# Performance work log

Measured on AMD Instinct MI355X. Metric: run time of the kernel, lower is better.

## Reference

```python
import jax, jax.numpy as jnp
import numpy as np

NUM_HEADS = 16


def _bayes_w(mu, rho, eps):
    # reparameterized weight sample: w = mu + softplus(rho) * eps
    return mu + jax.nn.softplus(rho) * eps


def setup_inputs() -> dict:
    key = jax.random.key(0)
    ks = jax.random.split(key, 12)
    B, N, C = 4, 2048, 1024
    x = jax.random.normal(ks[0], (B, N, C), jnp.float32)
    w_scale = 0.02
    q_w = jax.random.normal(ks[1], (C, C), jnp.float32) * w_scale
    k_w = jax.random.normal(ks[2], (C, C), jnp.float32) * w_scale
    v_mu = jax.random.normal(ks[3], (C, C), jnp.float32) * w_scale
    v_rho = jax.random.normal(ks[4], (C, C), jnp.float32) * 0.1 - 3.0
    v_eps = jax.random.normal(ks[5], (C, C), jnp.float32)
    proj_mu = jax.random.normal(ks[6], (C, C), jnp.float32) * w_scale
    proj_rho = jax.random.normal(ks[7], (C, C), jnp.float32) * 0.1 - 3.0
    proj_eps = jax.random.normal(ks[8], (C, C), jnp.float32)
    pb_mu = jax.random.normal(ks[9], (C,), jnp.float32) * w_scale
    pb_rho = jax.random.normal(ks[10], (C,), jnp.float32) * 0.1 - 3.0
    pb_eps = jax.random.normal(ks[11], (C,), jnp.float32)
    return {"x": x, "q_w": q_w, "k_w": k_w, "v_mu": v_mu, "v_rho": v_rho,
            "v_eps": v_eps, "proj_mu": proj_mu, "proj_rho": proj_rho,
            "proj_eps": proj_eps, "pb_mu": pb_mu, "pb_rho": pb_rho,
            "pb_eps": pb_eps}


def reference(x, q_w, k_w, v_mu, v_rho, v_eps, proj_mu, proj_rho, proj_eps,
              pb_mu, pb_rho, pb_eps):
    B, N, C = x.shape
    H = NUM_HEADS
    D = C // H
    scale = D ** -0.5
    v_w = _bayes_w(v_mu, v_rho, v_eps)
    # projections (torch Linear: y = x @ W.T)
    q = (x @ q_w.T).reshape(B, N, H, D).transpose(0, 2, 1, 3)  # [B,H,N,D]
    k = (x @ k_w.T).reshape(B, N, H, D).transpose(0, 2, 1, 3)
    v = (x @ v_w.T).reshape(B, N, H, D).transpose(0, 2, 1, 3)
    attn = jax.nn.softmax(jnp.einsum("bhnd,bhmd->bhnm", q * scale, k), axis=-1)
    out = jnp.einsum("bhnm,bhmd->bhnd", attn, v)
    out = out.transpose(0, 2, 1, 3).reshape(B, N, C)
    p_w = _bayes_w(proj_mu, proj_rho, proj_eps)
    p_b = _bayes_w(pb_mu, pb_rho, pb_eps)
    return out @ p_w.T + p_b
```

## Files before the change

### kernel.cpp

```cpp
#include <hip/hip_runtime.h>
#include <hip/hip_bf16.h>
#include <cstdint>
#include <math.h>

typedef __bf16 bf16;
typedef __bf16 bf16x8 __attribute__((ext_vector_type(8)));
typedef __bf16 bf16x4 __attribute__((ext_vector_type(4)));
typedef float  f32x4 __attribute__((ext_vector_type(4)));

#define LOG2E 1.4426950408889634f

#if __has_builtin(__builtin_amdgcn_exp2f)
#define EXP2(x) __builtin_amdgcn_exp2f(x)
#else
#define EXP2(x) exp2f(x)
#endif

#define AS1 __attribute__((address_space(1)))
#define AS3 __attribute__((address_space(3)))

__device__ __forceinline__ void gload_lds16(const bf16* g, bf16* l) {
    __builtin_amdgcn_global_load_lds((AS1 void*)g, (AS3 void*)l, 16, 0, 0);
}

__device__ __forceinline__ float softplus_f(float r) {
    return (r > 15.f) ? r : log1pf(expf(r));
}

#define MFMA16(a, b, c) __builtin_amdgcn_mfma_f32_16x16x32_bf16((a), (b), (c), 0, 0, 0)
#define CFENCE asm volatile("" ::: "memory")

__global__ __launch_bounds__(256)
void prep_kernel(const float* __restrict__ x, bf16* __restrict__ xb,
                 const float* __restrict__ q_w, const float* __restrict__ k_w,
                 bf16* __restrict__ wqkv,
                 const float* __restrict__ v_mu, const float* __restrict__ v_rho,
                 const float* __restrict__ v_eps,
                 const float* __restrict__ p_mu, const float* __restrict__ p_rho,
                 const float* __restrict__ p_eps, bf16* __restrict__ pwb,
                 const float* __restrict__ pb_mu, const float* __restrict__ pb_rho,
                 const float* __restrict__ pb_eps, float* __restrict__ p_b) {
    const int Wsz = 1024 * 1024;
    int blk = blockIdx.x;
    if (blk < 8192) {
        int i = blk * 256 + threadIdx.x;
        float4 v = ((const float4*)x)[i];
        bf16 o[4] = {(bf16)v.x, (bf16)v.y, (bf16)v.z, (bf16)v.w};
        *(uint64_t*)&xb[i * 4] = *(uint64_t*)o;
    } else if (blk < 10240) {
        const float* src = (blk < 9216) ? q_w : k_w;
        bf16* dst = (blk < 9216) ? wqkv : wqkv + Wsz;
        int i = ((blk - 8192) & 1023) * 256 + threadIdx.x;
        float4 v = ((const float4*)src)[i];
        bf16 o[4] = {(bf16)v.x, (bf16)v.y, (bf16)v.z, (bf16)v.w};
        *(uint64_t*)&dst[i * 4] = *(uint64_t*)o;
    } else if (blk < 12288) {
        const bool isv = blk < 11264;
        const float* mu  = isv ? v_mu  : p_mu;
        const float* rho = isv ? v_rho : p_rho;
        const float* eps = isv ? v_eps : p_eps;
        bf16* dst = isv ? wqkv + 2 * Wsz : pwb;
        int i = ((blk - 10240) & 1023) * 256 + threadIdx.x;
        float4 m = ((const float4*)mu)[i];
        float4 r = ((const float4*)rho)[i];
        float4 e = ((const float4*)eps)[i];
        bf16 o[4] = {(bf16)(m.x + softplus_f(r.x) * e.x),
                     (bf16)(m.y + softplus_f(r.y) * e.y),
                     (bf16)(m.z + softplus_f(r.z) * e.z),
                     (bf16)(m.w + softplus_f(r.w) * e.w)};
        *(uint64_t*)&dst[i * 4] = *(uint64_t*)o;
    } else {
        int i = threadIdx.x;
        float4 m = ((const float4*)pb_mu)[i];
        float4 r = ((const float4*)pb_rho)[i];
        float4 e = ((const float4*)pb_eps)[i];
        float4 o;
        o.x = m.x + softplus_f(r.x) * e.x;
        o.y = m.y + softplus_f(r.y) * e.y;
        o.z = m.z + softplus_f(r.z) * e.z;
        o.w = m.w + softplus_f(r.w) * e.w;
        ((float4*)p_b)[i] = o;
    }
}

template <typename OutT>
__global__ __launch_bounds__(512, 2)
void gemm_8ph(const bf16* __restrict__ A, const bf16* __restrict__ W,
              OutT* __restrict__ C, const float* __restrict__ bias,
              int M, int N, int K, float q_scale, int q_cols) {
    __shared__ bf16 sA[2][256 * 64];
    __shared__ bf16 sB[2][256 * 64];

    const int lane  = threadIdx.x & 63;
    const int wv    = threadIdx.x >> 6;
    const int wr    = wv >> 2;
    const int wc    = wv & 3;
    const int col16 = lane & 15, quad = lane >> 4;

    const int nwg = gridDim.x * gridDim.y;
    int bidl = blockIdx.y * gridDim.x + blockIdx.x;
    if ((nwg & 7) == 0) bidl = (bidl & 7) * (nwg >> 3) + (bidl >> 3);
    const int m0 = (bidl / gridDim.x) * 256;
    const int n0 = (bidl % gridDim.x) * 256;

    const int st_r = lane >> 2;
    const int st_c = ((lane & 3) * 8) ^ (((lane >> 5) & 1) << 4);
    const bf16* Asrc = A + (size_t)(m0 + st_r) * K + st_c;
    const bf16* Bsrc = W + (size_t)(n0 + st_r) * K + st_c;
    const size_t rgK = (size_t)16 * K;

    const int lp = col16 * 32 + ((quad * 8) ^ (((col16 >> 3) & 1) << 4));

    f32x4 acc[2][2][4][2] = {};
    const int NT = K >> 6;

    {
        const bf16* sa0 = Asrc + (size_t)wv * rgK;
        const bf16* sb0 = Bsrc + (size_t)wv * rgK;
        const bf16* sa1 = Asrc + (size_t)(8 + wv) * rgK;
        const bf16* sb1 = Bsrc + (size_t)(8 + wv) * rgK;
        gload_lds16(sa0,      &sA[0][wv * 1024]);        gload_lds16(sa0 + 32, &sA[0][wv * 1024 + 512]);
        gload_lds16(sb0,      &sB[0][wv * 1024]);        gload_lds16(sb0 + 32, &sB[0][wv * 1024 + 512]);
        gload_lds16(sa1,      &sA[0][(8+wv) * 1024]);    gload_lds16(sa1 + 32, &sA[0][(8+wv) * 1024 + 512]);
        gload_lds16(sb1,      &sB[0][(8+wv) * 1024]);    gload_lds16(sb1 + 32, &sB[0][(8+wv) * 1024 + 512]);
        gload_lds16(sa0 + 64, &sA[1][wv * 1024]);        gload_lds16(sa0 + 96, &sA[1][wv * 1024 + 512]);
        gload_lds16(sb0 + 64, &sB[1][wv * 1024]);        gload_lds16(sb0 + 96, &sB[1][wv * 1024 + 512]);
    }
    asm volatile("s_waitcnt vmcnt(4)" ::: "memory");
    __builtin_amdgcn_s_barrier();
    CFENCE;

    for (int t = 0; t < NT; ++t) {
        const int d = t & 1;
        const int k1 = (t + 1) << 6, k2 = (t + 2) << 6;
        bf16x8 afr[4][2], bfr[2][2];

#pragma unroll
        for (int mm = 0; mm < 4; ++mm)
#pragma unroll
            for (int ks = 0; ks < 2; ++ks)
                afr[mm][ks] = *(const bf16x8*)&sA[d][((2*mm + wr) * 2 + ks) * 512 + lp];
#pragma unroll
        for (int nn = 0; nn < 2; ++nn)
#pragma unroll
            for (int ks = 0; ks < 2; ++ks)
                bfr[nn][ks] = *(const bf16x8*)&sB[d][((nn*4 + wc) * 2 + ks) * 512 + lp];
        if (t + 1 < NT) {
            const bf16* s = Asrc + (size_t)(8 + wv) * rgK + k1;
            bf16* l = &sA[d ^ 1][(8 + wv) * 1024];
            gload_lds16(s, l); gload_lds16(s + 32, l + 512);
        }
        __builtin_amdgcn_s_setprio(1);
#pragma unroll
        for (int mm = 0; mm < 4; ++mm)
#pragma unroll
            for (int nn = 0; nn < 2; ++nn) {
                acc[0][0][mm][nn] = MFMA16(afr[mm][0], bfr[nn][0], acc[0][0][mm][nn]);
                acc[0][0][mm][nn] = MFMA16(afr[mm][1], bfr[nn][1], acc[0][0][mm][nn]);
            }
        __builtin_amdgcn_s_setprio(0);
        CFENCE; __builtin_amdgcn_s_barrier(); CFENCE;

#pragma unroll
        for (int nn = 0; nn < 2; ++nn)
#pragma unroll
            for (int ks = 0; ks < 2; ++ks)
                bfr[nn][ks] = *(const bf16x8*)&sB[d][((8 + nn*4 + wc) * 2 + ks) * 512 + lp];
        if (t + 1 < NT) {
            const bf16* s = Bsrc + (size_t)(8 + wv) * rgK + k1;
            bf16* l = &sB[d ^ 1][(8 + wv) * 1024];
            gload_lds16(s, l); gload_lds16(s + 32, l + 512);
        }
        __builtin_amdgcn_s_setprio(1);
#pragma unroll
        for (int mm = 0; mm < 4; ++mm)
#pragma unroll
            for (int nn = 0; nn < 2; ++nn) {
                acc[0][1][mm][nn] = MFMA16(afr[mm][0], bfr[nn][0], acc[0][1][mm][nn]);
                acc[0][1][mm][nn] = MFMA16(afr[mm][1], bfr[nn][1], acc[0][1][mm][nn]);
            }
        __builtin_amdgcn_s_setprio(0);
        CFENCE; __builtin_amdgcn_s_barrier(); CFENCE;

#pragma unroll
        for (int mm = 0; mm < 4; ++mm)
#pragma unroll
            for (int ks = 0; ks < 2; ++ks)
                afr[mm][ks] = *(const bf16x8*)&sA[d][((8 + 2*mm + wr) * 2 + ks) * 512 + lp];
#pragma unroll
        for (int nn = 0; nn < 2; ++nn)
#pragma unroll
            for (int ks = 0; ks < 2; ++ks)
                bfr[nn][ks] = *(const bf16x8*)&sB[d][((nn*4 + wc) * 2 + ks) * 512 + lp];
        if (t + 2 < NT) {
            const bf16* s = Asrc + (size_t)wv * rgK + k2;
            bf16* l = &sA[d][wv * 1024];
            gload_lds16(s, l); gload_lds16(s + 32, l + 512);
        }
        __builtin_amdgcn_s_setprio(1);
#pragma unroll
        for (int mm = 0; mm < 4; ++mm)
#pragma unroll
            for (int nn = 0; nn < 2; ++nn) {
                acc[1][0][mm][nn] = MFMA16(afr[mm][0], bfr[nn][0], acc[1][0][mm][nn]);
                acc[1][0][mm][nn] = MFMA16(afr[mm][1], bfr[nn][1], acc[1][0][mm][nn]);
            }
        __builtin_amdgcn_s_setprio(0);
        CFENCE; __builtin_amdgcn_s_barrier(); CFENCE;

#pragma unroll
        for (int nn = 0; nn < 2; ++nn)
#pragma unroll
            for (int ks = 0; ks < 2; ++ks)
                bfr[nn][ks] = *(const bf16x8*)&sB[d][((8 + nn*4 + wc) * 2 + ks) * 512 + lp];
        if (t + 2 < NT) {
            const bf16* s = Bsrc + (size_t)wv * rgK + k2;
            bf16* l = &sB[d][wv * 1024];
            gload_lds16(s, l); gload_lds16(s + 32, l + 512);
        }
        __builtin_amdgcn_s_setprio(1);
#pragma unroll
        for (int mm = 0; mm < 4; ++mm)
#pragma unroll
            for (int nn = 0; nn < 2; ++nn) {
                acc[1][1][mm][nn] = MFMA16(afr[mm][0], bfr[nn][0], acc[1][1][mm][nn]);
                acc[1][1][mm][nn] = MFMA16(afr[mm][1], bfr[nn][1], acc[1][1][mm][nn]);
            }
        __builtin_amdgcn_s_setprio(0);
        if (t + 2 < NT) asm volatile("s_waitcnt vmcnt(4)" ::: "memory");
        else            asm volatile("s_waitcnt vmcnt(0)" ::: "memory");
        __builtin_amdgcn_s_barrier();
        CFENCE;
    }

    const float scale = (n0 < q_cols) ? q_scale : 1.0f;
#pragma unroll
    for (int a = 0; a < 2; ++a)
#pragma unroll
        for (int b = 0; b < 2; ++b)
#pragma unroll
            for (int mm = 0; mm < 4; ++mm)
#pragma unroll
                for (int nn = 0; nn < 2; ++nn) {
                    int row = m0 + (a * 8 + 2 * mm + wr) * 16 + quad * 4;
                    int cc  = n0 + (b * 8 + nn * 4 + wc) * 16 + col16;
                    float bv = bias ? bias[cc] : 0.f;
#pragma unroll
                    for (int r = 0; r < 4; ++r)
                        C[(size_t)(row + r) * N + cc] = (OutT)(acc[a][b][mm][nn][r] * scale + bv);
                }
}

#define SWZ(row, ec) ((row) * 64 + ((ec) ^ (((row) & 7) << 3)))

__global__ __launch_bounds__(256, 2)
void attn_kernel(const bf16* __restrict__ QKV, bf16* __restrict__ O) {
    __shared__ bf16 sK[2][64 * 64];
    __shared__ bf16 sVt[64 * 64];
    __shared__ bf16 sP [256 * 64];

    const int lane = threadIdx.x & 63;
    const int wv   = threadIdx.x >> 6;
    const int col  = lane & 15, quad = lane >> 4;

    const int bid  = blockIdx.x;
    const int work = (bid & 7) * 64 + (bid >> 3);
    const int qt = work & 7, h = (work >> 3) & 15, b = work >> 7;

    const size_t rowQ0 = (size_t)b * 2048 + qt * 256;
    const bf16* Qg = QKV + rowQ0 * 3072 + h * 64;
    const bf16* Kg = QKV + (size_t)b * 2048 * 3072 + 1024 + h * 64;
    const bf16* Vg = QKV + (size_t)b * 2048 * 3072 + 2048 + h * 64;

    const int rloc = lane >> 3;
    const bf16* Kdma = Kg + (size_t)(wv * 16 + rloc) * 3072 + (((lane & 7) ^ rloc) * 8);

    gload_lds16(Kdma,                    &sK[0][(wv * 16) * 64]);
    gload_lds16(Kdma + (size_t)8 * 3072, &sK[0][(wv * 16 + 8) * 64]);

    const int dc0 = wv * 8, dc1 = 32 + wv * 8;
    bf16x8 vr0 = *(const bf16x8*)&Vg[(size_t)lane * 3072 + dc0];
    bf16x8 vr1 = *(const bf16x8*)&Vg[(size_t)lane * 3072 + dc1];

#pragma unroll
    for (int it = 0; it < 8; ++it) {
        int c = it * 256 + threadIdx.x;
        int row = c >> 3, ec = (c & 7) * 8;
        *(bf16x8*)&sP[SWZ(row, ec)] = *(const bf16x8*)&Qg[(size_t)row * 3072 + ec];
    }
    __syncthreads();
    bf16x8 qf[4][2];
#pragma unroll
    for (int mi = 0; mi < 4; ++mi)
#pragma unroll
        for (int ks = 0; ks < 2; ++ks)
            qf[mi][ks] = *(const bf16x8*)&sP[SWZ(wv * 64 + mi * 16 + col, ks * 32 + quad * 8)];

    f32x4 lsum[4] = {};
    f32x4 o[4][4] = {};
    const int cx = col & 7;

    for (int t = 0; t < 32; ++t) {
        const int p = t & 1;

#pragma unroll
        for (int j = 0; j < 8; ++j) sVt[SWZ(dc0 + j, lane)] = vr0[j];
#pragma unroll
        for (int j = 0; j < 8; ++j) sVt[SWZ(dc1 + j, lane)] = vr1[j];
        __syncthreads();

        if (t < 31) {
            const bf16* kn = Kdma + (size_t)(t * 64 + 64) * 3072;
            gload_lds16(kn,                    &sK[p ^ 1][(wv * 16) * 64]);
            gload_lds16(kn + (size_t)8 * 3072, &sK[p ^ 1][(wv * 16 + 8) * 64]);
        }

        bf16x8 kf0[4], kf1[4];
#pragma unroll
        for (int nj = 0; nj < 4; ++nj) {
            kf0[nj] = *(const bf16x8*)&sK[p][(nj * 16 + col) * 64 + ((quad ^ cx) * 8)];
            kf1[nj] = *(const bf16x8*)&sK[p][(nj * 16 + col) * 64 + (((quad ^ cx) ^ 4) * 8)];
        }

#pragma unroll
        for (int mi = 0; mi < 4; ++mi) {
            f32x4 st[4];
            __builtin_amdgcn_s_setprio(1);
#pragma unroll
            for (int nj = 0; nj < 4; ++nj) {
                f32x4 tacc = {0.f, 0.f, 0.f, 0.f};
                tacc = MFMA16(kf0[nj], qf[mi][0], tacc);
                tacc = MFMA16(kf1[nj], qf[mi][1], tacc);
                st[nj] = tacc;
            }
            __builtin_amdgcn_s_setprio(0);
#pragma unroll
            for (int nj = 0; nj < 4; ++nj) {
                f32x4 pv;
#pragma unroll
                for (int r = 0; r < 4; ++r) pv[r] = EXP2(st[nj][r]);
                lsum[mi] += pv;
                bf16x4 pk = {(bf16)pv[0], (bf16)pv[1], (bf16)pv[2], (bf16)pv[3]};
                *(bf16x4*)&sP[SWZ(wv * 64 + mi * 16 + col, nj * 16 + quad * 4)] = pk;
            }
        }

        if (t < 31) {
            const bf16* vn = Vg + (size_t)(t * 64 + 64 + lane) * 3072;
            vr0 = *(const bf16x8*)&vn[dc0];
            vr1 = *(const bf16x8*)&vn[dc1];
        }

        __builtin_amdgcn_s_setprio(1);
#pragma unroll
        for (int ks = 0; ks < 2; ++ks) {
            bf16x8 pf[4];
#pragma unroll
            for (int mi = 0; mi < 4; ++mi)
                pf[mi] = *(const bf16x8*)&sP[SWZ(wv * 64 + mi * 16 + col, ks * 32 + quad * 8)];
#pragma unroll
            for (int dj = 0; dj < 4; ++dj) {
                bf16x8 vf = *(const bf16x8*)&sVt[SWZ(dj * 16 + col, ks * 32 + quad * 8)];
#pragma unroll
                for (int mi = 0; mi < 4; ++mi)
                    o[mi][dj] = MFMA16(pf[mi], vf, o[mi][dj]);
            }
        }
        __builtin_amdgcn_s_setprio(0);
        __syncthreads();
    }

#pragma unroll
    for (int mi = 0; mi < 4; ++mi) {
        float l = lsum[mi][0] + lsum[mi][1] + lsum[mi][2] + lsum[mi][3];
        l += __shfl_xor(l, 16, 64);
        l += __shfl_xor(l, 32, 64);
#pragma unroll
        for (int r = 0; r < 4; ++r) {
            float inv = 1.f / __shfl(l, quad * 4 + r, 64);
            size_t row = rowQ0 + wv * 64 + mi * 16 + quad * 4 + r;
#pragma unroll
            for (int dj = 0; dj < 4; ++dj)
                O[row * 1024 + h * 64 + dj * 16 + col] = (bf16)(o[mi][dj][r] * inv);
        }
    }
}

extern "C" void kernel_launch(void* const* d_in, const int* in_sizes, int n_in,
                              void* d_out, int out_size, void* d_ws, size_t ws_size,
                              hipStream_t stream) {
    const float* x      = (const float*)d_in[0];
    const float* q_w    = (const float*)d_in[1];
    const float* k_w    = (const float*)d_in[2];
    const float* v_mu   = (const float*)d_in[3];
    const float* v_rho  = (const float*)d_in[4];
    const float* v_eps  = (const float*)d_in[5];
    const float* p_mu   = (const float*)d_in[6];
    const float* p_rho  = (const float*)d_in[7];
    const float* p_eps  = (const float*)d_in[8];
    const float* pb_mu  = (const float*)d_in[9];
    const float* pb_rho = (const float*)d_in[10];
    const float* pb_eps = (const float*)d_in[11];
    float* out = (float*)d_out;

    const size_t MB = (size_t)1 << 20;
    char* ws = (char*)d_ws;
    bf16*  xb   = (bf16*)(ws);
    bf16*  wqkv = (bf16*)(ws + 16 * MB);
    bf16*  pwb  = (bf16*)(ws + 22 * MB);
    float* p_b  = (float*)(ws + 24 * MB);
    bf16*  QKV  = (bf16*)(ws + 25 * MB);
    bf16*  Ab   = xb;

    prep_kernel<<<12289, 256, 0, stream>>>(x, xb, q_w, k_w, wqkv,
                                           v_mu, v_rho, v_eps,
                                           p_mu, p_rho, p_eps, pwb,
                                           pb_mu, pb_rho, pb_eps, p_b);

    gemm_8ph<bf16><<<dim3(12, 32), 512, 0, stream>>>(xb, wqkv, QKV, nullptr,
                                                     8192, 3072, 1024, 0.125f * LOG2E, 1024);

    attn_kernel<<<dim3(512), 256, 0, stream>>>(QKV, Ab);

    gemm_8ph<float><<<dim3(4, 32), 512, 0, stream>>>(Ab, pwb, out, p_b,
                                                     8192, 1024, 1024, 1.0f, 1024);
}
```

Measured before the change: 302.7 us.

## Reuse B fragments across quadrants and reorder GEMM LDS prefetch stages

Restructures the 256x256 GEMM main loop so the two B-fragment sets are kept in registers and reused across the four sub-tile MFMA blocks. This removes two of the four B LDS reloads per K-step. The quadrant order becomes 00, 01, 11, 10, and global-to-LDS prefetches are rescheduled one quarter at a time, with an extra barrier after each issue and a deeper vmcnt(6) wait. The cost is more live registers and an extra barrier per phase.

```diff
diff --git a/kernel.cpp b/kernel.cpp
--- a/kernel.cpp
+++ b/kernel.cpp
@@ -114,49 +114,46 @@
     f32x4 acc[2][2][4][2] = {};
     const int NT = K >> 6;
 
-    {
-        const bf16* sa0 = Asrc + (size_t)wv * rgK;
-        const bf16* sb0 = Bsrc + (size_t)wv * rgK;
-        const bf16* sa1 = Asrc + (size_t)(8 + wv) * rgK;
-        const bf16* sb1 = Bsrc + (size_t)(8 + wv) * rgK;
-        gload_lds16(sa0,      &sA[0][wv * 1024]);        gload_lds16(sa0 + 32, &sA[0][wv * 1024 + 512]);
-        gload_lds16(sb0,      &sB[0][wv * 1024]);        gload_lds16(sb0 + 32, &sB[0][wv * 1024 + 512]);
-        gload_lds16(sa1,      &sA[0][(8+wv) * 1024]);    gload_lds16(sa1 + 32, &sA[0][(8+wv) * 1024 + 512]);
-        gload_lds16(sb1,      &sB[0][(8+wv) * 1024]);    gload_lds16(sb1 + 32, &sB[0][(8+wv) * 1024 + 512]);
-        gload_lds16(sa0 + 64, &sA[1][wv * 1024]);        gload_lds16(sa0 + 96, &sA[1][wv * 1024 + 512]);
-        gload_lds16(sb0 + 64, &sB[1][wv * 1024]);        gload_lds16(sb0 + 96, &sB[1][wv * 1024 + 512]);
-    }
-    asm volatile("s_waitcnt vmcnt(4)" ::: "memory");
+#define STAGE_A(buf, half, kt) do { \
+        const bf16* s_ = Asrc + (size_t)((half) * 8 + wv) * rgK + ((size_t)(kt) << 6); \
+        bf16* l_ = &sA[buf][((half) * 8 + wv) * 1024]; \
+        gload_lds16(s_, l_); gload_lds16(s_ + 32, l_ + 512); } while (0)
+#define STAGE_B(buf, half, kt) do { \
+        const bf16* s_ = Bsrc + (size_t)((half) * 8 + wv) * rgK + ((size_t)(kt) << 6); \
+        bf16* l_ = &sB[buf][((half) * 8 + wv) * 1024]; \
+        gload_lds16(s_, l_); gload_lds16(s_ + 32, l_ + 512); } while (0)
+
+    STAGE_A(0, 0, 0); STAGE_B(0, 0, 0); STAGE_B(0, 1, 0); STAGE_A(0, 1, 0);
+    if (NT > 1) { STAGE_A(1, 0, 1); STAGE_B(1, 0, 1); STAGE_B(1, 1, 1); }
+    if (NT > 1) asm volatile("s_waitcnt vmcnt(6)" ::: "memory");
+    else        asm volatile("s_waitcnt vmcnt(0)" ::: "memory");
     __builtin_amdgcn_s_barrier();
     CFENCE;
 
+    bf16x8 afr[4][2], bfr0[2][2], bfr1[2][2];
+
     for (int t = 0; t < NT; ++t) {
         const int d = t & 1;
-        const int k1 = (t + 1) << 6, k2 = (t + 2) << 6;
-        bf16x8 afr[4][2], bfr[2][2];
 
 #pragma unroll
         for (int mm = 0; mm < 4; ++mm)
 #pragma unroll
             for (int ks = 0; ks < 2; ++ks)
-                afr[mm][ks] = *(const bf16x8*)&sA[d][((2*mm + wr) * 2 + ks) * 512 + lp];
+                afr[mm][ks] = *(const bf16x8*)&sA[d][((2 * mm + wr) * 2 + ks) * 512 + lp];
 #pragma unroll
         for (int nn = 0; nn < 2; ++nn)
 #pragma unroll
             for (int ks = 0; ks < 2; ++ks)
-                bfr[nn][ks] = *(const bf16x8*)&sB[d][((nn*4 + wc) * 2 + ks) * 512 + lp];
-        if (t + 1 < NT) {
-            const bf16* s = Asrc + (size_t)(8 + wv) * rgK + k1;
-            bf16* l = &sA[d ^ 1][(8 + wv) * 1024];
-            gload_lds16(s, l); gload_lds16(s + 32, l + 512);
-        }
+                bfr0[nn][ks] = *(const bf16x8*)&sB[d][((nn * 4 + wc) * 2 + ks) * 512 + lp];
+        if (t + 1 < NT) STAGE_A(d ^ 1, 1, t + 1);
+        CFENCE; __builtin_amdgcn_s_barrier(); CFENCE;
         __builtin_amdgcn_s_setprio(1);
 #pragma unroll
         for (int mm = 0; mm < 4; ++mm)
 #pragma unroll
             for (int nn = 0; nn < 2; ++nn) {
-                acc[0][0][mm][nn] = MFMA16(afr[mm][0], bfr[nn][0], acc[0][0][mm][nn]);
-                acc[0][0][mm][nn] = MFMA16(afr[mm][1], bfr[nn][1], acc[0][0][mm][nn]);
+                acc[0][0][mm][nn] = MFMA16(afr[mm][0], bfr0[nn][0], acc[0][0][mm][nn]);
+                acc[0][0][mm][nn] = MFMA16(afr[mm][1], bfr0[nn][1], acc[0][0][mm][nn]);
             }
         __builtin_amdgcn_s_setprio(0);
         CFENCE; __builtin_amdgcn_s_barrier(); CFENCE;
@@ -165,19 +162,16 @@
         for (int nn = 0; nn < 2; ++nn)
 #pragma unroll
             for (int ks = 0; ks < 2; ++ks)
-                bfr[nn][ks] = *(const bf16x8*)&sB[d][((8 + nn*4 + wc) * 2 + ks) * 512 + lp];
-        if (t + 1 < NT) {
-            const bf16* s = Bsrc + (size_t)(8 + wv) * rgK + k1;
-            bf16* l = &sB[d ^ 1][(8 + wv) * 1024];
-            gload_lds16(s, l); gload_lds16(s + 32, l + 512);
-        }
+                bfr1[nn][ks] = *(const bf16x8*)&sB[d][((8 + nn * 4 + wc) * 2 + ks) * 512 + lp];
+        if (t + 2 < NT) STAGE_A(d, 0, t + 2);
+        CFENCE; __builtin_amdgcn_s_barrier(); CFENCE;
         __builtin_amdgcn_s_setprio(1);
 #pragma unroll
         for (int mm = 0; mm < 4; ++mm)
 #pragma unroll
             for (int nn = 0; nn < 2; ++nn) {
-                acc[0][1][mm][nn] = MFMA16(afr[mm][0], bfr[nn][0], acc[0][1][mm][nn]);
-                acc[0][1][mm][nn] = MFMA16(afr[mm][1], bfr[nn][1], acc[0][1][mm][nn]);
+                acc[0][1][mm][nn] = MFMA16(afr[mm][0], bfr1[nn][0], acc[0][1][mm][nn]);
+                acc[0][1][mm][nn] = MFMA16(afr[mm][1], bfr1[nn][1], acc[0][1][mm][nn]);
             }
         __builtin_amdgcn_s_setprio(0);
         CFENCE; __builtin_amdgcn_s_barrier(); CFENCE;
@@ -186,52 +180,38 @@
         for (int mm = 0; mm < 4; ++mm)
 #pragma unroll
             for (int ks = 0; ks < 2; ++ks)
-                afr[mm][ks] = *(const bf16x8*)&sA[d][((8 + 2*mm + wr) * 2 + ks) * 512 + lp];
-#pragma unroll
-        for (int nn = 0; nn < 2; ++nn)
-#pragma unroll
-            for (int ks = 0; ks < 2; ++ks)
-                bfr[nn][ks] = *(const bf16x8*)&sB[d][((nn*4 + wc) * 2 + ks) * 512 + lp];
-        if (t + 2 < NT) {
-            const bf16* s = Asrc + (size_t)wv * rgK + k2;
-            bf16* l = &sA[d][wv * 1024];
-            gload_lds16(s, l); gload_lds16(s + 32, l + 512);
-        }
+                afr[mm][ks] = *(const bf16x8*)&sA[d][((8 + 2 * mm + wr) * 2 + ks) * 512 + lp];
+        if (t + 2 < NT) STAGE_B(d, 0, t + 2);
+        CFENCE; __builtin_amdgcn_s_barrier(); CFENCE;
         __builtin_amdgcn_s_setprio(1);
 #pragma unroll
         for (int mm = 0; mm < 4; ++mm)
 #pragma unroll
             for (int nn = 0; nn < 2; ++nn) {
-                acc[1][0][mm][nn] = MFMA16(afr[mm][0], bfr[nn][0], acc[1][0][mm][nn]);
-                acc[1][0][mm][nn] = MFMA16(afr[mm][1], bfr[nn][1], acc[1][0][mm][nn]);
+                acc[1][1][mm][nn] = MFMA16(afr[mm][0], bfr1[nn][0], acc[1][1][mm][nn]);
+                acc[1][1][mm][nn] = MFMA16(afr[mm][1], bfr1[nn][1], acc[1][1][mm][nn]);
             }
         __builtin_amdgcn_s_setprio(0);
         CFENCE; __builtin_amdgcn_s_barrier(); CFENCE;
 
-#pragma unroll
-        for (int nn = 0; nn < 2; ++nn)
-#pragma unroll
-            for (int ks = 0; ks < 2; ++ks)
-                bfr[nn][ks] = *(const bf16x8*)&sB[d][((8 + nn*4 + wc) * 2 + ks) * 512 + lp];
-        if (t + 2 < NT) {
-            const bf16* s = Bsrc + (size_t)wv * rgK + k2;
-            bf16* l = &sB[d][wv * 1024];
-            gload_lds16(s, l); gload_lds16(s + 32, l + 512);
-        }
+        if (t + 2 < NT) STAGE_B(d, 1, t + 2);
+        CFENCE; __builtin_amdgcn_s_barrier(); CFENCE;
         __builtin_amdgcn_s_setprio(1);
 #pragma unroll
         for (int mm = 0; mm < 4; ++mm)
 #pragma unroll
             for (int nn = 0; nn < 2; ++nn) {
-                acc[1][1][mm][nn] = MFMA16(afr[mm][0], bfr[nn][0], acc[1][1][mm][nn]);
-                acc[1][1][mm][nn] = MFMA16(afr[mm][1], bfr[nn][1], acc[1][1][mm][nn]);
+                acc[1][0][mm][nn] = MFMA16(afr[mm][0], bfr0[nn][0], acc[1][0][mm][nn]);
+                acc[1][0][mm][nn] = MFMA16(afr[mm][1], bfr0[nn][1], acc[1][0][mm][nn]);
             }
         __builtin_amdgcn_s_setprio(0);
-        if (t + 2 < NT) asm volatile("s_waitcnt vmcnt(4)" ::: "memory");
+        if (t + 2 < NT) asm volatile("s_waitcnt vmcnt(6)" ::: "memory");
         else            asm volatile("s_waitcnt vmcnt(0)" ::: "memory");
         __builtin_amdgcn_s_barrier();
         CFENCE;
     }
+#undef STAGE_A
+#undef STAGE_B
 
     const float scale = (n0 < q_cols) ? q_scale : 1.0f;
 #pragma unroll
```

After: 304.8 us. Within noise of the previous version (+0.7%).
